# Optimization experiments

Measured on AMD Instinct MI355X. Metric: run time of the kernel, lower is better.

Reference implementation:

```python
import jax, jax.numpy as jnp
import numpy as np

B = 131072  # batch of states
D = 32      # input/hidden width (hardcoded in Policy)
L = 40      # number of hidden layers

def setup_inputs() -> dict:
    key = jax.random.key(0)
    k1, k2, k3, k4, k5 = jax.random.split(key, 5)
    scale = 1.0 / np.sqrt(D)  # ~ torch Linear init scale
    return {
        "state": jax.random.normal(k1, (B, D), dtype=jnp.float32),
        "W_hidden": jax.random.normal(k2, (L, D, D), dtype=jnp.float32) * scale,
        "b_hidden": jax.random.normal(k3, (L, D), dtype=jnp.float32) * scale,
        "W_out": jax.random.normal(k4, (1, D), dtype=jnp.float32) * scale,
        "b_out": jax.random.normal(k5, (1,), dtype=jnp.float32) * scale,
    }

def reference(state, W_hidden, b_hidden, W_out, b_out):
    # torch Linear: y = x @ W.T + b, with W of shape [out, in].
    def layer(x, wb):
        w, b = wb
        return jax.nn.relu(jnp.einsum('bi,oi->bo', x, w) + b), None
    x, _ = jax.lax.scan(layer, state, (W_hidden, b_hidden))
    # final Linear(32, 1), no activation
    return jnp.einsum('bi,oi->bo', x, W_out) + b_out  # [B, 1]
```

## Files before the change

kernel.cpp:

```cpp
#include <hip/hip_runtime.h>


#define NB 131072
#define DD 32
#define NL 40
#define WTAB_BYTES ((NL + 1) * 4 * 64 * 16)

typedef short bf16x8 __attribute__((ext_vector_type(8)));
typedef float f32x16 __attribute__((ext_vector_type(16)));

union Frag { int4 q; int i[4]; bf16x8 v; };

__device__ inline unsigned f2bf(float f) {
  unsigned u = __float_as_uint(f);
  return (u + 0x7fffu + ((u >> 16) & 1u)) >> 16;
}
__device__ inline float bf2f(unsigned s) { return __int_as_float((int)(s << 16)); }

__global__ __launch_bounds__(64) void build_tables(
    const float* __restrict__ Wh, const float* __restrict__ bh,
    const float* __restrict__ Wout, const float* __restrict__ bout,
    int4* __restrict__ wtab, int* __restrict__ btab) {
  const int l = blockIdx.x;
  const int lane = threadIdx.x;
  const int m = lane & 31, h = lane >> 5;
  for (int g = 0; g < 4; ++g) {
    const int kk = g & 1;
    const bool lopart = (g >= 2);
    int wds[4];
    for (int w = 0; w < 4; ++w) {
      const int k = 16 * kk + 8 * (w >> 1) + 4 * h + 2 * (w & 1);
      float a, b;
      if (l < NL) {
        a = Wh[(l * 32 + m) * 32 + k];
        b = Wh[(l * 32 + m) * 32 + k + 1];
      } else {
        a = (m == 0) ? Wout[k] : 0.f;
        b = (m == 0) ? Wout[k + 1] : 0.f;
      }
      unsigned ah = f2bf(a), bhh = f2bf(b);
      unsigned al = f2bf(a - bf2f(ah)), bl = f2bf(b - bf2f(bhh));
      wds[w] = lopart ? (int)(al | (bl << 16)) : (int)(ah | (bhh << 16));
    }
    wtab[(l * 4 + g) * 64 + lane] = make_int4(wds[0], wds[1], wds[2], wds[3]);
  }
  float bv = (l < NL) ? bh[l * 32 + m] : ((m == 0) ? bout[0] : 0.f);
  unsigned bhi = f2bf(bv);
  unsigned blo = f2bf(bv - bf2f(bhi));
  btab[l * 64 + lane] = (h == 0) ? (int)(bhi | (blo << 16)) : 0;
}

__device__ inline int cvt_pk(float a, float b) {
  int r;
  asm("v_cvt_pk_bf16_f32 %0, %1, %2" : "=v"(r) : "v"(a), "v"(b));
  return r;
}
__device__ inline void split2(float a, float b, int& hi, int& lo) {
  hi = cvt_pk(a, b);
  float ha = __int_as_float(hi << 16);
  float hb = __int_as_float(hi & (int)0xffff0000u);
  lo = cvt_pk(a - ha, b - hb);
}

__global__ __launch_bounds__(256) void policy_mfma(
    const float* __restrict__ state, const int4* __restrict__ wtab,
    const int* __restrict__ btab, float* __restrict__ out) {
  const int lane = threadIdx.x & 63;
  const int wid = (int)((blockIdx.x * blockDim.x + threadIdx.x) >> 6);
  const int n = lane & 31, h = lane >> 5;
  const int bbase = wid * 32;

  Frag bhi0, bhi1, blo0, blo1;
  {
    const float* xr = state + (size_t)(bbase + n) * DD;
    float4 xa = *(const float4*)(xr + 4 * h);
    float4 xb = *(const float4*)(xr + 8 + 4 * h);
    float4 xc = *(const float4*)(xr + 16 + 4 * h);
    float4 xd = *(const float4*)(xr + 24 + 4 * h);
    split2(xa.x, xa.y, bhi0.i[0], blo0.i[0]);
    split2(xa.z, xa.w, bhi0.i[1], blo0.i[1]);
    split2(xb.x, xb.y, bhi0.i[2], blo0.i[2]);
    split2(xb.z, xb.w, bhi0.i[3], blo0.i[3]);
    split2(xc.x, xc.y, bhi1.i[0], blo1.i[0]);
    split2(xc.z, xc.w, bhi1.i[1], blo1.i[1]);
    split2(xd.x, xd.y, bhi1.i[2], blo1.i[2]);
    split2(xd.z, xd.w, bhi1.i[3], blo1.i[3]);
  }

  Frag bones;
  bones.i[0] = (h == 0) ? 0x3F803F80 : 0;
  bones.i[1] = bones.i[2] = bones.i[3] = 0;

  Frag ab;
  ab.i[1] = ab.i[2] = ab.i[3] = 0;

  const f32x16 zero16 = {0, 0, 0, 0, 0, 0, 0, 0, 0, 0, 0, 0, 0, 0, 0, 0};

  const int4* wp = wtab + lane;
  const int* bp = btab + lane;
  int4 nw0 = wp[0], nw1 = wp[64], nw2 = wp[128], nw3 = wp[192];
  int nb = bp[0];

  float result = 0.f;

#pragma unroll 1
  for (int l = 0; l <= NL; ++l) {
    Frag wh0, wh1, wl0, wl1;
    wh0.q = nw0; wh1.q = nw1; wl0.q = nw2; wl1.q = nw3;
    ab.i[0] = nb;
    if (l < NL) {
      wp += 256; bp += 64;
      nw0 = wp[0]; nw1 = wp[64]; nw2 = wp[128]; nw3 = wp[192];
      nb = bp[0];
    }

    f32x16 acc = __builtin_amdgcn_mfma_f32_32x32x16_bf16(ab.v, bones.v, zero16, 0, 0, 0);
    acc = __builtin_amdgcn_mfma_f32_32x32x16_bf16(wh0.v, bhi0.v, acc, 0, 0, 0);
    acc = __builtin_amdgcn_mfma_f32_32x32x16_bf16(wl0.v, bhi0.v, acc, 0, 0, 0);
    acc = __builtin_amdgcn_mfma_f32_32x32x16_bf16(wh1.v, bhi1.v, acc, 0, 0, 0);
    acc = __builtin_amdgcn_mfma_f32_32x32x16_bf16(wl1.v, bhi1.v, acc, 0, 0, 0);
    acc = __builtin_amdgcn_mfma_f32_32x32x16_bf16(wh0.v, blo0.v, acc, 0, 0, 0);
    acc = __builtin_amdgcn_mfma_f32_32x32x16_bf16(wh1.v, blo1.v, acc, 0, 0, 0);

    if (l < NL) {
#pragma unroll
      for (int p = 0; p < 8; ++p) {
        float a = fmaxf(acc[2 * p], 0.f);
        float b = fmaxf(acc[2 * p + 1], 0.f);
        int hi, lo;
        split2(a, b, hi, lo);
        if (p < 4) { bhi0.i[p] = hi; blo0.i[p] = lo; }
        else       { bhi1.i[p - 4] = hi; blo1.i[p - 4] = lo; }
      }
    } else {
      result = acc[0];
    }
  }

  if (h == 0) out[bbase + n] = result;
}

extern "C" void kernel_launch(void* const* d_in, const int* in_sizes, int n_in,
                              void* d_out, int out_size, void* d_ws, size_t ws_size,
                              hipStream_t stream) {
  const float* state = (const float*)d_in[0];
  const float* Wh    = (const float*)d_in[1];
  const float* bh    = (const float*)d_in[2];
  const float* Wout  = (const float*)d_in[3];
  const float* bout  = (const float*)d_in[4];
  float* out = (float*)d_out;

  int4* wtab = (int4*)d_ws;
  int* btab  = (int*)((char*)d_ws + WTAB_BYTES);

  build_tables<<<NL + 1, 64, 0, stream>>>(Wh, bh, Wout, bout, wtab, btab);

  policy_mfma<<<(NB / 32) * 64 / 256, 256, 0, stream>>>(state, wtab, btab, out);
}
```

Baseline: 52.12 us.

## Process two 32-row tiles per wave with interleaved independent MFMA chains

Each wavefront now handles 64 batch rows as two independent 32-row tiles. It interleaves their MFMA accumulation chains so that one chain's latency can hide behind the other's, and it reuses the loaded weight fragments across both tiles. The grid is halved and launch bounds now state one block minimum. The cost is roughly double the register pressure per wave and half as many waves in flight, which can reduce latency hiding from occupancy.

```diff
diff --git a/kernel.cpp b/kernel.cpp
--- a/kernel.cpp
+++ b/kernel.cpp
@@ -62,29 +62,32 @@
   lo = cvt_pk(a - ha, b - hb);
 }
 
-__global__ __launch_bounds__(256) void policy_mfma(
+#define MFMA(A, B, C) __builtin_amdgcn_mfma_f32_32x32x16_bf16((A), (B), (C), 0, 0, 0)
+
+__global__ __launch_bounds__(256, 1) void policy_mfma(
     const float* __restrict__ state, const int4* __restrict__ wtab,
     const int* __restrict__ btab, float* __restrict__ out) {
   const int lane = threadIdx.x & 63;
   const int wid = (int)((blockIdx.x * blockDim.x + threadIdx.x) >> 6);
   const int n = lane & 31, h = lane >> 5;
-  const int bbase = wid * 32;
+  const int bbase = wid * 64;
 
-  Frag bhi0, bhi1, blo0, blo1;
-  {
-    const float* xr = state + (size_t)(bbase + n) * DD;
+  Frag bhi0[2], bhi1[2], blo0[2], blo1[2];
+#pragma unroll
+  for (int t = 0; t < 2; ++t) {
+    const float* xr = state + (size_t)(bbase + 32 * t + n) * DD;
     float4 xa = *(const float4*)(xr + 4 * h);
     float4 xb = *(const float4*)(xr + 8 + 4 * h);
     float4 xc = *(const float4*)(xr + 16 + 4 * h);
     float4 xd = *(const float4*)(xr + 24 + 4 * h);
-    split2(xa.x, xa.y, bhi0.i[0], blo0.i[0]);
-    split2(xa.z, xa.w, bhi0.i[1], blo0.i[1]);
-    split2(xb.x, xb.y, bhi0.i[2], blo0.i[2]);
-    split2(xb.z, xb.w, bhi0.i[3], blo0.i[3]);
-    split2(xc.x, xc.y, bhi1.i[0], blo1.i[0]);
-    split2(xc.z, xc.w, bhi1.i[1], blo1.i[1]);
-    split2(xd.x, xd.y, bhi1.i[2], blo1.i[2]);
-    split2(xd.z, xd.w, bhi1.i[3], blo1.i[3]);
+    split2(xa.x, xa.y, bhi0[t].i[0], blo0[t].i[0]);
+    split2(xa.z, xa.w, bhi0[t].i[1], blo0[t].i[1]);
+    split2(xb.x, xb.y, bhi0[t].i[2], blo0[t].i[2]);
+    split2(xb.z, xb.w, bhi0[t].i[3], blo0[t].i[3]);
+    split2(xc.x, xc.y, bhi1[t].i[0], blo1[t].i[0]);
+    split2(xc.z, xc.w, bhi1[t].i[1], blo1[t].i[1]);
+    split2(xd.x, xd.y, bhi1[t].i[2], blo1[t].i[2]);
+    split2(xd.z, xd.w, bhi1[t].i[3], blo1[t].i[3]);
   }
 
   Frag bones;
@@ -101,7 +104,7 @@
   int4 nw0 = wp[0], nw1 = wp[64], nw2 = wp[128], nw3 = wp[192];
   int nb = bp[0];
 
-  float result = 0.f;
+  float result[2] = {0.f, 0.f};
 
 #pragma unroll 1
   for (int l = 0; l <= NL; ++l) {
@@ -114,30 +117,44 @@
       nb = bp[0];
     }
 
-    f32x16 acc = __builtin_amdgcn_mfma_f32_32x32x16_bf16(ab.v, bones.v, zero16, 0, 0, 0);
-    acc = __builtin_amdgcn_mfma_f32_32x32x16_bf16(wh0.v, bhi0.v, acc, 0, 0, 0);
-    acc = __builtin_amdgcn_mfma_f32_32x32x16_bf16(wl0.v, bhi0.v, acc, 0, 0, 0);
-    acc = __builtin_amdgcn_mfma_f32_32x32x16_bf16(wh1.v, bhi1.v, acc, 0, 0, 0);
-    acc = __builtin_amdgcn_mfma_f32_32x32x16_bf16(wl1.v, bhi1.v, acc, 0, 0, 0);
-    acc = __builtin_amdgcn_mfma_f32_32x32x16_bf16(wh0.v, blo0.v, acc, 0, 0, 0);
-    acc = __builtin_amdgcn_mfma_f32_32x32x16_bf16(wh1.v, blo1.v, acc, 0, 0, 0);
+    f32x16 a0 = MFMA(ab.v, bones.v, zero16);
+    f32x16 a1 = MFMA(ab.v, bones.v, zero16);
+    a0 = MFMA(wh0.v, bhi0[0].v, a0);
+    a1 = MFMA(wh0.v, bhi0[1].v, a1);
+    a0 = MFMA(wl0.v, bhi0[0].v, a0);
+    a1 = MFMA(wl0.v, bhi0[1].v, a1);
+    a0 = MFMA(wh1.v, bhi1[0].v, a0);
+    a1 = MFMA(wh1.v, bhi1[1].v, a1);
+    a0 = MFMA(wl1.v, bhi1[0].v, a0);
+    a1 = MFMA(wl1.v, bhi1[1].v, a1);
+    a0 = MFMA(wh0.v, blo0[0].v, a0);
+    a1 = MFMA(wh0.v, blo0[1].v, a1);
+    a0 = MFMA(wh1.v, blo1[0].v, a0);
+    a1 = MFMA(wh1.v, blo1[1].v, a1);
 
     if (l < NL) {
 #pragma unroll
       for (int p = 0; p < 8; ++p) {
-        float a = fmaxf(acc[2 * p], 0.f);
-        float b = fmaxf(acc[2 * p + 1], 0.f);
+        float xa0 = fmaxf(a0[2 * p], 0.f), ya0 = fmaxf(a0[2 * p + 1], 0.f);
+        float xa1 = fmaxf(a1[2 * p], 0.f), ya1 = fmaxf(a1[2 * p + 1], 0.f);
         int hi, lo;
-        split2(a, b, hi, lo);
-        if (p < 4) { bhi0.i[p] = hi; blo0.i[p] = lo; }
-        else       { bhi1.i[p - 4] = hi; blo1.i[p - 4] = lo; }
+        split2(xa0, ya0, hi, lo);
+        if (p < 4) { bhi0[0].i[p] = hi; blo0[0].i[p] = lo; }
+        else       { bhi1[0].i[p - 4] = hi; blo1[0].i[p - 4] = lo; }
+        split2(xa1, ya1, hi, lo);
+        if (p < 4) { bhi0[1].i[p] = hi; blo0[1].i[p] = lo; }
+        else       { bhi1[1].i[p - 4] = hi; blo1[1].i[p - 4] = lo; }
       }
     } else {
-      result = acc[0];
+      result[0] = a0[0];
+      result[1] = a1[0];
     }
   }
 
-  if (h == 0) out[bbase + n] = result;
+  if (h == 0) {
+    out[bbase + n] = result[0];
+    out[bbase + 32 + n] = result[1];
+  }
 }
 
 extern "C" void kernel_launch(void* const* d_in, const int* in_sizes, int n_in,
@@ -155,5 +172,5 @@
 
   build_tables<<<NL + 1, 64, 0, stream>>>(Wh, bh, Wout, bout, wtab, btab);
 
-  policy_mfma<<<(NB / 32) * 64 / 256, 256, 0, stream>>>(state, wtab, btab, out);
+  policy_mfma<<<(NB / 64) * 64 / 256, 256, 0, stream>>>(state, wtab, btab, out);
 }
```

Measured after the change: 54.90 us. 5.3% more time.

## Switch per-layer MFMA to 16x16x32 tiles with fp32 bias as accumulator init

Applied to the files above, without the earlier changes.

Replaces the chain of seven dependent 32x32x16 bf16 MFMAs per layer with twelve 16x16x32 MFMAs arranged as four independent accumulator chains. The bias is now loaded in fp32 as the initial accumulator, which removes the extra bias MFMA and the bf16 hi/lo bias split. The weight and bias tables are rebuilt to match the 16x16 fragment layout, and launch bounds now request 4 blocks per CU. The goal is to shorten the dependent MFMA latency chain per layer and expose more instruction-level parallelism, at the cost of more MFMA instructions issued.

```diff
diff --git a/kernel.cpp b/kernel.cpp
--- a/kernel.cpp
+++ b/kernel.cpp
@@ -7,9 +7,10 @@
 #define WTAB_BYTES ((NL + 1) * 4 * 64 * 16)
 
 typedef short bf16x8 __attribute__((ext_vector_type(8)));
-typedef float f32x16 __attribute__((ext_vector_type(16)));
+typedef float f32x4 __attribute__((ext_vector_type(4)));
 
 union Frag { int4 q; int i[4]; bf16x8 v; };
+union BFrag { float4 q; f32x4 v; };
 
 __device__ inline unsigned f2bf(float f) {
   unsigned u = __float_as_uint(f);
@@ -20,34 +21,38 @@
 __global__ __launch_bounds__(64) void build_tables(
     const float* __restrict__ Wh, const float* __restrict__ bh,
     const float* __restrict__ Wout, const float* __restrict__ bout,
-    int4* __restrict__ wtab, int* __restrict__ btab) {
+    int4* __restrict__ wtab, float4* __restrict__ btab) {
   const int l = blockIdx.x;
   const int lane = threadIdx.x;
-  const int m = lane & 31, h = lane >> 5;
-  for (int g = 0; g < 4; ++g) {
-    const int kk = g & 1;
-    const bool lopart = (g >= 2);
+  const int m = lane & 15, g = lane >> 4;
+  for (int p = 0; p < 4; ++p) {
+    const int row = (p & 1) ? (16 + m) : m;
+    const bool lopart = (p >= 2);
     int wds[4];
     for (int w = 0; w < 4; ++w) {
-      const int k = 16 * kk + 8 * (w >> 1) + 4 * h + 2 * (w & 1);
-      float a, b;
-      if (l < NL) {
-        a = Wh[(l * 32 + m) * 32 + k];
-        b = Wh[(l * 32 + m) * 32 + k + 1];
-      } else {
-        a = (m == 0) ? Wout[k] : 0.f;
-        b = (m == 0) ? Wout[k + 1] : 0.f;
+      unsigned wd = 0;
+      for (int e = 0; e < 2; ++e) {
+        const int j = 2 * w + e;
+        const int k = (j < 4) ? (4 * g + j) : (16 + 4 * g + (j - 4));
+        float v;
+        if (l < NL) v = Wh[(l * 32 + row) * 32 + k];
+        else        v = (row == 0) ? Wout[k] : 0.f;
+        unsigned hi = f2bf(v);
+        unsigned val = lopart ? f2bf(v - bf2f(hi)) : hi;
+        wd |= val << (16 * e);
       }
-      unsigned ah = f2bf(a), bhh = f2bf(b);
-      unsigned al = f2bf(a - bf2f(ah)), bl = f2bf(b - bf2f(bhh));
-      wds[w] = lopart ? (int)(al | (bl << 16)) : (int)(ah | (bhh << 16));
+      wds[w] = (int)wd;
     }
-    wtab[(l * 4 + g) * 64 + lane] = make_int4(wds[0], wds[1], wds[2], wds[3]);
+    wtab[(l * 4 + p) * 64 + lane] = make_int4(wds[0], wds[1], wds[2], wds[3]);
   }
-  float bv = (l < NL) ? bh[l * 32 + m] : ((m == 0) ? bout[0] : 0.f);
-  unsigned bhi = f2bf(bv);
-  unsigned blo = f2bf(bv - bf2f(bhi));
-  btab[l * 64 + lane] = (h == 0) ? (int)(bhi | (blo << 16)) : 0;
+  for (int a = 0; a < 2; ++a) {
+    float bv[4];
+    for (int r = 0; r < 4; ++r) {
+      const int row = 16 * a + 4 * g + r;
+      bv[r] = (l < NL) ? bh[l * 32 + row] : ((row == 0) ? bout[0] : 0.f);
+    }
+    btab[(l * 2 + a) * 64 + lane] = make_float4(bv[0], bv[1], bv[2], bv[3]);
+  }
 }
 
 __device__ inline int cvt_pk(float a, float b) {
@@ -62,82 +67,79 @@
   lo = cvt_pk(a - ha, b - hb);
 }
 
-__global__ __launch_bounds__(256) void policy_mfma(
+#define MFMA16(A, B, C) __builtin_amdgcn_mfma_f32_16x16x32_bf16((A), (B), (C), 0, 0, 0)
+
+__global__ __launch_bounds__(256, 4) void policy_mfma(
     const float* __restrict__ state, const int4* __restrict__ wtab,
-    const int* __restrict__ btab, float* __restrict__ out) {
+    const float4* __restrict__ btab, float* __restrict__ out) {
   const int lane = threadIdx.x & 63;
   const int wid = (int)((blockIdx.x * blockDim.x + threadIdx.x) >> 6);
-  const int n = lane & 31, h = lane >> 5;
+  const int n = lane & 15, g = lane >> 4;
   const int bbase = wid * 32;
 
-  Frag bhi0, bhi1, blo0, blo1;
-  {
-    const float* xr = state + (size_t)(bbase + n) * DD;
-    float4 xa = *(const float4*)(xr + 4 * h);
-    float4 xb = *(const float4*)(xr + 8 + 4 * h);
-    float4 xc = *(const float4*)(xr + 16 + 4 * h);
-    float4 xd = *(const float4*)(xr + 24 + 4 * h);
-    split2(xa.x, xa.y, bhi0.i[0], blo0.i[0]);
-    split2(xa.z, xa.w, bhi0.i[1], blo0.i[1]);
-    split2(xb.x, xb.y, bhi0.i[2], blo0.i[2]);
-    split2(xb.z, xb.w, bhi0.i[3], blo0.i[3]);
-    split2(xc.x, xc.y, bhi1.i[0], blo1.i[0]);
-    split2(xc.z, xc.w, bhi1.i[1], blo1.i[1]);
-    split2(xd.x, xd.y, bhi1.i[2], blo1.i[2]);
-    split2(xd.z, xd.w, bhi1.i[3], blo1.i[3]);
+  Frag bhi[2], blo[2];
+#pragma unroll
+  for (int t = 0; t < 2; ++t) {
+    const float* xr = state + (size_t)(bbase + 16 * t + n) * DD;
+    float4 xa = *(const float4*)(xr + 4 * g);
+    float4 xc = *(const float4*)(xr + 16 + 4 * g);
+    split2(xa.x, xa.y, bhi[t].i[0], blo[t].i[0]);
+    split2(xa.z, xa.w, bhi[t].i[1], blo[t].i[1]);
+    split2(xc.x, xc.y, bhi[t].i[2], blo[t].i[2]);
+    split2(xc.z, xc.w, bhi[t].i[3], blo[t].i[3]);
   }
 
-  Frag bones;
-  bones.i[0] = (h == 0) ? 0x3F803F80 : 0;
-  bones.i[1] = bones.i[2] = bones.i[3] = 0;
+  const int4* wp = wtab + lane;
+  const float4* bp = btab + lane;
+  int4 nw0h = wp[0], nw1h = wp[64], nw0l = wp[128], nw1l = wp[192];
+  float4 nb0 = bp[0], nb1 = bp[64];
 
-  Frag ab;
-  ab.i[1] = ab.i[2] = ab.i[3] = 0;
-
-  const f32x16 zero16 = {0, 0, 0, 0, 0, 0, 0, 0, 0, 0, 0, 0, 0, 0, 0, 0};
-
-  const int4* wp = wtab + lane;
-  const int* bp = btab + lane;
-  int4 nw0 = wp[0], nw1 = wp[64], nw2 = wp[128], nw3 = wp[192];
-  int nb = bp[0];
-
-  float result = 0.f;
+  float res0 = 0.f, res1 = 0.f;
 
 #pragma unroll 1
   for (int l = 0; l <= NL; ++l) {
-    Frag wh0, wh1, wl0, wl1;
-    wh0.q = nw0; wh1.q = nw1; wl0.q = nw2; wl1.q = nw3;
-    ab.i[0] = nb;
+    Frag w0h, w1h, w0l, w1l;
+    w0h.q = nw0h; w1h.q = nw1h; w0l.q = nw0l; w1l.q = nw1l;
+    BFrag c0, c1;
+    c0.q = nb0; c1.q = nb1;
     if (l < NL) {
-      wp += 256; bp += 64;
-      nw0 = wp[0]; nw1 = wp[64]; nw2 = wp[128]; nw3 = wp[192];
-      nb = bp[0];
+      wp += 256; bp += 128;
+      nw0h = wp[0]; nw1h = wp[64]; nw0l = wp[128]; nw1l = wp[192];
+      nb0 = bp[0]; nb1 = bp[64];
     }
 
-    f32x16 acc = __builtin_amdgcn_mfma_f32_32x32x16_bf16(ab.v, bones.v, zero16, 0, 0, 0);
-    acc = __builtin_amdgcn_mfma_f32_32x32x16_bf16(wh0.v, bhi0.v, acc, 0, 0, 0);
-    acc = __builtin_amdgcn_mfma_f32_32x32x16_bf16(wl0.v, bhi0.v, acc, 0, 0, 0);
-    acc = __builtin_amdgcn_mfma_f32_32x32x16_bf16(wh1.v, bhi1.v, acc, 0, 0, 0);
-    acc = __builtin_amdgcn_mfma_f32_32x32x16_bf16(wl1.v, bhi1.v, acc, 0, 0, 0);
-    acc = __builtin_amdgcn_mfma_f32_32x32x16_bf16(wh0.v, blo0.v, acc, 0, 0, 0);
-    acc = __builtin_amdgcn_mfma_f32_32x32x16_bf16(wh1.v, blo1.v, acc, 0, 0, 0);
+    f32x4 a00 = MFMA16(w0h.v, bhi[0].v, c0.v);
+    f32x4 a01 = MFMA16(w1h.v, bhi[0].v, c1.v);
+    f32x4 a10 = MFMA16(w0h.v, bhi[1].v, c0.v);
+    f32x4 a11 = MFMA16(w1h.v, bhi[1].v, c1.v);
+    a00 = MFMA16(w0l.v, bhi[0].v, a00);
+    a01 = MFMA16(w1l.v, bhi[0].v, a01);
+    a10 = MFMA16(w0l.v, bhi[1].v, a10);
+    a11 = MFMA16(w1l.v, bhi[1].v, a11);
+    a00 = MFMA16(w0h.v, blo[0].v, a00);
+    a01 = MFMA16(w1h.v, blo[0].v, a01);
+    a10 = MFMA16(w0h.v, blo[1].v, a10);
+    a11 = MFMA16(w1h.v, blo[1].v, a11);
 
     if (l < NL) {
-#pragma unroll
-      for (int p = 0; p < 8; ++p) {
-        float a = fmaxf(acc[2 * p], 0.f);
-        float b = fmaxf(acc[2 * p + 1], 0.f);
-        int hi, lo;
-        split2(a, b, hi, lo);
-        if (p < 4) { bhi0.i[p] = hi; blo0.i[p] = lo; }
-        else       { bhi1.i[p - 4] = hi; blo1.i[p - 4] = lo; }
-      }
+      split2(fmaxf(a00[0], 0.f), fmaxf(a00[1], 0.f), bhi[0].i[0], blo[0].i[0]);
+      split2(fmaxf(a00[2], 0.f), fmaxf(a00[3], 0.f), bhi[0].i[1], blo[0].i[1]);
+      split2(fmaxf(a01[0], 0.f), fmaxf(a01[1], 0.f), bhi[0].i[2], blo[0].i[2]);
+      split2(fmaxf(a01[2], 0.f), fmaxf(a01[3], 0.f), bhi[0].i[3], blo[0].i[3]);
+      split2(fmaxf(a10[0], 0.f), fmaxf(a10[1], 0.f), bhi[1].i[0], blo[1].i[0]);
+      split2(fmaxf(a10[2], 0.f), fmaxf(a10[3], 0.f), bhi[1].i[1], blo[1].i[1]);
+      split2(fmaxf(a11[0], 0.f), fmaxf(a11[1], 0.f), bhi[1].i[2], blo[1].i[2]);
+      split2(fmaxf(a11[2], 0.f), fmaxf(a11[3], 0.f), bhi[1].i[3], blo[1].i[3]);
     } else {
-      result = acc[0];
+      res0 = a00[0];
+      res1 = a10[0];
     }
   }
 
-  if (h == 0) out[bbase + n] = result;
+  if (lane < 16) {
+    out[bbase + n] = res0;
+    out[bbase + 16 + n] = res1;
+  }
 }
 
 extern "C" void kernel_launch(void* const* d_in, const int* in_sizes, int n_in,
@@ -151,7 +153,7 @@
   float* out = (float*)d_out;
 
   int4* wtab = (int4*)d_ws;
-  int* btab  = (int*)((char*)d_ws + WTAB_BYTES);
+  float4* btab = (float4*)((char*)d_ws + WTAB_BYTES);
 
   build_tables<<<NL + 1, 64, 0, stream>>>(Wh, bh, Wout, bout, wtab, btab);
 
```

After: 53.68 us. +3.0%, slower.

## Stage weight tables in LDS, unroll layer loop, truncate-split activations

Applied to the files above, without the earlier changes.

Copies the compacted bias table and the first 38 layers of pre-split bf16 weight fragments into LDS at block start, with 1024-thread blocks, so per-layer weight loads come from shared memory rather than global/L2. The layer loop is fully unrolled with double-buffered weight fragments, and the output layer is peeled. The hi/lo split now uses truncation via byte-permute instead of round-to-nearest conversion. The bias table is also compacted to 32 entries per layer. The trade-offs are a large LDS allocation (about 160 KB per block), which limits occupancy to one block of 16 waves per CU and adds a block-wide copy and barrier up front, plus larger code from the unroll. The truncating split also shifts rounding of the high part.

```diff
diff --git a/kernel.cpp b/kernel.cpp
--- a/kernel.cpp
+++ b/kernel.cpp
@@ -4,7 +4,10 @@
 #define NB 131072
 #define DD 32
 #define NL 40
-#define WTAB_BYTES ((NL + 1) * 4 * 64 * 16)
+#define BIAS_BYTES ((NL + 1) * 32 * 4)
+#define WTAB_OFF   BIAS_BYTES
+#define LDS_LAYERS 38
+#define LDS_BYTES  (BIAS_BYTES + LDS_LAYERS * 4096)
 
 typedef short bf16x8 __attribute__((ext_vector_type(8)));
 typedef float f32x16 __attribute__((ext_vector_type(16)));
@@ -20,10 +23,12 @@
 __global__ __launch_bounds__(64) void build_tables(
     const float* __restrict__ Wh, const float* __restrict__ bh,
     const float* __restrict__ Wout, const float* __restrict__ bout,
-    int4* __restrict__ wtab, int* __restrict__ btab) {
+    char* __restrict__ ws) {
   const int l = blockIdx.x;
   const int lane = threadIdx.x;
   const int m = lane & 31, h = lane >> 5;
+  int4* wtab = (int4*)(ws + WTAB_OFF);
+  int* bc = (int*)ws;
   for (int g = 0; g < 4; ++g) {
     const int kk = g & 1;
     const bool lopart = (g >= 2);
@@ -44,31 +49,41 @@
     }
     wtab[(l * 4 + g) * 64 + lane] = make_int4(wds[0], wds[1], wds[2], wds[3]);
   }
-  float bv = (l < NL) ? bh[l * 32 + m] : ((m == 0) ? bout[0] : 0.f);
-  unsigned bhi = f2bf(bv);
-  unsigned blo = f2bf(bv - bf2f(bhi));
-  btab[l * 64 + lane] = (h == 0) ? (int)(bhi | (blo << 16)) : 0;
+  if (lane < 32) {
+    float bv = (l < NL) ? bh[l * 32 + lane] : ((lane == 0) ? bout[0] : 0.f);
+    unsigned bhi = f2bf(bv);
+    unsigned blo = f2bf(bv - bf2f(bhi));
+    bc[l * 32 + lane] = (int)(bhi | (blo << 16));
+  }
 }
 
-__device__ inline int cvt_pk(float a, float b) {
-  int r;
-  asm("v_cvt_pk_bf16_f32 %0, %1, %2" : "=v"(r) : "v"(a), "v"(b));
-  return r;
-}
 __device__ inline void split2(float a, float b, int& hi, int& lo) {
-  hi = cvt_pk(a, b);
-  float ha = __int_as_float(hi << 16);
-  float hb = __int_as_float(hi & (int)0xffff0000u);
-  lo = cvt_pk(a - ha, b - hb);
+  const unsigned ia = __float_as_uint(a), ib = __float_as_uint(b);
+  hi = (int)__builtin_amdgcn_perm(ia, ib, 0x03020706u);
+  const float ha = __int_as_float((int)(ia & 0xffff0000u));
+  const float hb = __int_as_float((int)(ib & 0xffff0000u));
+  const float la = a - ha, lb = b - hb;
+  lo = (int)__builtin_amdgcn_perm(__float_as_uint(la), __float_as_uint(lb),
+                                  0x03020706u);
 }
 
-__global__ __launch_bounds__(256) void policy_mfma(
-    const float* __restrict__ state, const int4* __restrict__ wtab,
-    const int* __restrict__ btab, float* __restrict__ out) {
-  const int lane = threadIdx.x & 63;
-  const int wid = (int)((blockIdx.x * blockDim.x + threadIdx.x) >> 6);
+#define MFMA32(A, B, C) __builtin_amdgcn_mfma_f32_32x32x16_bf16((A), (B), (C), 0, 0, 0)
+
+__global__ __launch_bounds__(1024, 4) void policy_mfma(
+    const float* __restrict__ state, const char* __restrict__ tab,
+    float* __restrict__ out) {
+  extern __shared__ char smem[];
+  const int tid = threadIdx.x;
+  const int lane = tid & 63;
   const int n = lane & 31, h = lane >> 5;
+  const int wid = blockIdx.x * 16 + (tid >> 6);
   const int bbase = wid * 32;
+
+  {
+    const int4* src = (const int4*)tab;
+    int4* dst = (int4*)smem;
+    for (int i = tid; i < LDS_BYTES / 16; i += 1024) dst[i] = src[i];
+  }
 
   Frag bhi0, bhi1, blo0, blo1;
   {
@@ -90,54 +105,76 @@
   Frag bones;
   bones.i[0] = (h == 0) ? 0x3F803F80 : 0;
   bones.i[1] = bones.i[2] = bones.i[3] = 0;
+  const int hmask = (h == 0) ? -1 : 0;
 
-  Frag ab;
-  ab.i[1] = ab.i[2] = ab.i[3] = 0;
+  __syncthreads();
+
+  const int4* lw = (const int4*)(smem + WTAB_OFF) + lane;
+  const int* bc = (const int*)smem;
+  const int4* gw = (const int4*)(tab + WTAB_OFF) + lane;
 
   const f32x16 zero16 = {0, 0, 0, 0, 0, 0, 0, 0, 0, 0, 0, 0, 0, 0, 0, 0};
 
-  const int4* wp = wtab + lane;
-  const int* bp = btab + lane;
-  int4 nw0 = wp[0], nw1 = wp[64], nw2 = wp[128], nw3 = wp[192];
-  int nb = bp[0];
+  Frag Wf[2][4];
+  int nb[2];
+  Wf[0][0].q = lw[0];
+  Wf[0][1].q = lw[64];
+  Wf[0][2].q = lw[128];
+  Wf[0][3].q = lw[192];
+  nb[0] = bc[n];
 
-  float result = 0.f;
+#pragma unroll
+  for (int l = 0; l < NL; ++l) {
+    const int cur = l & 1, nxt = cur ^ 1;
 
-#pragma unroll 1
-  for (int l = 0; l <= NL; ++l) {
-    Frag wh0, wh1, wl0, wl1;
-    wh0.q = nw0; wh1.q = nw1; wl0.q = nw2; wl1.q = nw3;
-    ab.i[0] = nb;
-    if (l < NL) {
-      wp += 256; bp += 64;
-      nw0 = wp[0]; nw1 = wp[64]; nw2 = wp[128]; nw3 = wp[192];
-      nb = bp[0];
+    {
+      const int lp = l + 1;
+      const int4* src = (lp < LDS_LAYERS) ? lw : gw;
+      Wf[nxt][0].q = src[lp * 256 + 0];
+      Wf[nxt][1].q = src[lp * 256 + 64];
+      Wf[nxt][2].q = src[lp * 256 + 128];
+      Wf[nxt][3].q = src[lp * 256 + 192];
+      nb[nxt] = bc[lp * 32 + n];
     }
 
-    f32x16 acc = __builtin_amdgcn_mfma_f32_32x32x16_bf16(ab.v, bones.v, zero16, 0, 0, 0);
-    acc = __builtin_amdgcn_mfma_f32_32x32x16_bf16(wh0.v, bhi0.v, acc, 0, 0, 0);
-    acc = __builtin_amdgcn_mfma_f32_32x32x16_bf16(wl0.v, bhi0.v, acc, 0, 0, 0);
-    acc = __builtin_amdgcn_mfma_f32_32x32x16_bf16(wh1.v, bhi1.v, acc, 0, 0, 0);
-    acc = __builtin_amdgcn_mfma_f32_32x32x16_bf16(wl1.v, bhi1.v, acc, 0, 0, 0);
-    acc = __builtin_amdgcn_mfma_f32_32x32x16_bf16(wh0.v, blo0.v, acc, 0, 0, 0);
-    acc = __builtin_amdgcn_mfma_f32_32x32x16_bf16(wh1.v, blo1.v, acc, 0, 0, 0);
+    Frag ab;
+    ab.i[0] = nb[cur] & hmask;
+    ab.i[1] = ab.i[2] = ab.i[3] = 0;
+    f32x16 acc = MFMA32(ab.v, bones.v, zero16);
+    acc = MFMA32(Wf[cur][0].v, bhi0.v, acc);
+    acc = MFMA32(Wf[cur][2].v, bhi0.v, acc);
+    acc = MFMA32(Wf[cur][1].v, bhi1.v, acc);
+    acc = MFMA32(Wf[cur][3].v, bhi1.v, acc);
+    acc = MFMA32(Wf[cur][0].v, blo0.v, acc);
+    acc = MFMA32(Wf[cur][1].v, blo1.v, acc);
 
-    if (l < NL) {
 #pragma unroll
-      for (int p = 0; p < 8; ++p) {
-        float a = fmaxf(acc[2 * p], 0.f);
-        float b = fmaxf(acc[2 * p + 1], 0.f);
-        int hi, lo;
-        split2(a, b, hi, lo);
-        if (p < 4) { bhi0.i[p] = hi; blo0.i[p] = lo; }
-        else       { bhi1.i[p - 4] = hi; blo1.i[p - 4] = lo; }
-      }
-    } else {
-      result = acc[0];
+    for (int p = 0; p < 8; ++p) {
+      float a = fmaxf(acc[2 * p], 0.f);
+      float b = fmaxf(acc[2 * p + 1], 0.f);
+      int hi, lo;
+      split2(a, b, hi, lo);
+      if (p < 4) { bhi0.i[p] = hi; blo0.i[p] = lo; }
+      else       { bhi1.i[p - 4] = hi; blo1.i[p - 4] = lo; }
     }
   }
 
-  if (h == 0) out[bbase + n] = result;
+  float res;
+  {
+    Frag ab;
+    ab.i[0] = nb[0] & hmask;
+    ab.i[1] = ab.i[2] = ab.i[3] = 0;
+    f32x16 acc = MFMA32(ab.v, bones.v, zero16);
+    acc = MFMA32(Wf[0][0].v, bhi0.v, acc);
+    acc = MFMA32(Wf[0][2].v, bhi0.v, acc);
+    acc = MFMA32(Wf[0][1].v, bhi1.v, acc);
+    acc = MFMA32(Wf[0][3].v, bhi1.v, acc);
+    acc = MFMA32(Wf[0][0].v, blo0.v, acc);
+    acc = MFMA32(Wf[0][1].v, blo1.v, acc);
+    res = acc[0];
+  }
+
+  if (h == 0) out[bbase + n] = res;
 }
 
 extern "C" void kernel_launch(void* const* d_in, const int* in_sizes, int n_in,
@@ -150,10 +187,7 @@
   const float* bout  = (const float*)d_in[4];
   float* out = (float*)d_out;
 
-  int4* wtab = (int4*)d_ws;
-  int* btab  = (int*)((char*)d_ws + WTAB_BYTES);
+  build_tables<<<NL + 1, 64, 0, stream>>>(Wh, bh, Wout, bout, (char*)d_ws);
 
-  build_tables<<<NL + 1, 64, 0, stream>>>(Wh, bh, Wout, bout, wtab, btab);
-
-  policy_mfma<<<(NB / 32) * 64 / 256, 256, 0, stream>>>(state, wtab, btab, out);
+  policy_mfma<<<256, 1024, LDS_BYTES, stream>>>(state, (const char*)d_ws, out);
 }
```

Result: faster. 44.79 us (-14.1%).
